# Kernel tuning notes

Measured on AMD Instinct MI355X. Metric: run time of the kernel, lower is better.

## Reference

```python
import jax, jax.numpy as jnp
import numpy as np

GRID = (32, 32)
LATENT = 256
ALPHA = 1.0
DECAY = 0.9


def _cdist(a, b):
    # Euclidean pairwise distance with a grad-safe sqrt (0 where d2==0, like torch.cdist).
    d2 = jnp.sum(a * a, -1)[:, None] + jnp.sum(b * b, -1)[None, :] - 2.0 * (a @ b.T)
    d2 = jnp.maximum(d2, 0.0)
    mask = d2 > 0
    return jnp.where(mask, jnp.sqrt(jnp.where(mask, d2, 1.0)), 0.0)


def setup_inputs() -> dict:
    key = jax.random.key(0)
    k1, k2 = jax.random.split(key)
    z = jax.random.normal(k1, (64, 512, 256), dtype=jnp.float32)
    nodes = jax.random.normal(k2, (GRID[0], GRID[1], LATENT), dtype=jnp.float32)
    return {"z": z, "nodes": nodes}


def reference(z, nodes):
    b, t, d = z.shape
    # time_decay^(seq_len - t - 1)
    tw = DECAY ** (t - 1 - jnp.arange(t, dtype=jnp.float32))
    z_flat = (z * tw[None, :, None]).reshape(b * t, d)   # (b t) d
    nodes_flat = nodes.reshape(-1, d)                     # n d

    dist = _cdist(z_flat, nodes_flat)                     # (b t) n
    q = 1.0 / (1.0 + dist / ALPHA) ** ((ALPHA + 1.0) / 2.0)
    q = q / jnp.sum(q, axis=-1, keepdims=True)            # L1 normalize rows
    q2 = q * q
    p = q2 / jnp.sum(q2, axis=0, keepdims=True)
    p = p / jnp.sum(p, axis=-1, keepdims=True)

    bmu = jnp.argmin(dist, axis=-1).reshape(b, t)         # int32

    # F.kl_div(q.log(), p, reduction='batchmean') = sum(p*(log p - log q)) / N
    kl_loss = jnp.sum(p * (jnp.log(p) - jnp.log(q))) / (b * t)
    diversity_loss = -jnp.mean(_cdist(nodes_flat, nodes_flat))
    time_smooth_loss = jnp.mean((z[:, 1:] - z[:, :-1]) ** 2) * DECAY

    # vectorized neighborhood consistency (python loop in the original is an
    # unweighted mean over all (b, t) adjacent pairs since seq_len is uniform)
    gw = GRID[1]
    pc = jnp.stack([bmu[:, :-1] // gw, bmu[:, :-1] % gw], axis=-1)
    nc = jnp.stack([bmu[:, 1:] // gw, bmu[:, 1:] % gw], axis=-1)
    neighbor_loss = jnp.mean(jnp.sum(jnp.abs(pc - nc), axis=-1).astype(jnp.float32))

    total_loss = kl_loss + 0.5 * diversity_loss + 0.3 * time_smooth_loss + 0.2 * neighbor_loss

    bmu_nodes = nodes_flat[bmu.reshape(-1)].reshape(b, t, d)
    som_z = z + 0.1 * (bmu_nodes - z)
    return (som_z, total_loss, kl_loss, diversity_loss, time_smooth_loss, neighbor_loss, q, bmu)
```

## Files before the change

kernel.cpp:

```cpp
#include <hip/hip_runtime.h>
#include <math.h>

#define Bb 64
#define Tt 512
#define Dd 256
#define Nn 1024
#define NROWS 32768

#define OUT_SOM 0L
#define OUT_SCAL 8388608L
#define OUT_Q 8388613L
#define OUT_BMU 41943045L

typedef __attribute__((ext_vector_type(8))) short bf16x8;
typedef __attribute__((ext_vector_type(4))) float f32x4;
typedef unsigned long long u64;
typedef unsigned short ushortT;

static __device__ __forceinline__ unsigned short f2bf(float x) {
  unsigned int u = __float_as_uint(x);
  unsigned int r = (u + 0x7fffu + ((u >> 16) & 1u)) >> 16;
  return (unsigned short)r;
}
static __device__ __forceinline__ float bf2f(unsigned short b) {
  return __uint_as_float(((unsigned int)b) << 16);
}

static __device__ __forceinline__ float block_reduce_sum(float v, float* sb) {
#pragma unroll
  for (int o = 32; o > 0; o >>= 1) v += __shfl_down(v, o, 64);
  const int lane = threadIdx.x & 63, w = threadIdx.x >> 6;
  if (lane == 0) sb[w] = v;
  __syncthreads();
  return (threadIdx.x == 0) ? (sb[0] + sb[1] + sb[2] + sb[3]) : 0.0f;
}

__global__ __launch_bounds__(256) void k_conv(
    const float* __restrict__ z, const float* __restrict__ nodes,
    ushortT* __restrict__ zhiF, ushortT* __restrict__ zloF, float* __restrict__ zn,
    ushortT* __restrict__ nhiF, ushortT* __restrict__ nloF, float* __restrict__ nnorm) {
  __shared__ float sm[32 * 260];
  const int tid = threadIdx.x;
  if (blockIdx.x < 1024) {
    const int rt = blockIdx.x;
    const long row0 = (long)rt * 32;
    const int r = tid >> 3, c8 = tid & 7;
    const long rowg = row0 + r;
    const int t = (int)(rowg & (Tt - 1));
    const float tw = powf(0.9f, (float)(Tt - 1 - t));
    float nrm = 0.f;
#pragma unroll
    for (int k = 0; k < 8; ++k) {
      const int c4 = c8 + k * 8;
      float4 v = ((const float4*)(z + rowg * Dd))[c4];
      v.x *= tw; v.y *= tw; v.z *= tw; v.w *= tw;
      *(float4*)&sm[r * 260 + c4 * 4] = v;
      nrm += v.x * v.x + v.y * v.y + v.z * v.z + v.w * v.w;
    }
    nrm += __shfl_xor(nrm, 1, 64);
    nrm += __shfl_xor(nrm, 2, 64);
    nrm += __shfl_xor(nrm, 4, 64);
    if (c8 == 0) zn[rowg] = nrm;
    __syncthreads();
    ushort4* oh = (ushort4*)(zhiF + (long)rt * 8192);
    ushort4* ol = (ushort4*)(zloF + (long)rt * 8192);
#pragma unroll
    for (int i = 0; i < 8; ++i) {
      const int o4 = tid + 256 * i;
      const int e4 = (o4 & 1) * 4;
      const int r16 = (o4 >> 1) & 15;
      const int k8 = (o4 >> 5) & 3;
      const int g = (o4 >> 7) & 1;
      const int ks = o4 >> 8;
      const float* p = &sm[(g * 16 + r16) * 260 + ks * 32 + k8 * 8 + e4];
      const float4 v = *(const float4*)p;
      ushort4 h, l;
      h.x = f2bf(v.x); l.x = f2bf(v.x - bf2f(h.x));
      h.y = f2bf(v.y); l.y = f2bf(v.y - bf2f(h.y));
      h.z = f2bf(v.z); l.z = f2bf(v.z - bf2f(h.z));
      h.w = f2bf(v.w); l.w = f2bf(v.w - bf2f(h.w));
      oh[o4] = h;
      ol[o4] = l;
    }
  } else {
    const int ct = blockIdx.x - 1024;
    const int jr = tid >> 4, cg = tid & 15;
    const long nrow = (long)(ct * 16 + jr);
    float nrm = 0.f;
#pragma unroll
    for (int k = 0; k < 4; ++k) {
      const int c4 = cg + k * 16;
      const float4 v = ((const float4*)(nodes + nrow * Dd))[c4];
      *(float4*)&sm[jr * 260 + c4 * 4] = v;
      nrm += v.x * v.x + v.y * v.y + v.z * v.z + v.w * v.w;
    }
    nrm += __shfl_xor(nrm, 1, 64);
    nrm += __shfl_xor(nrm, 2, 64);
    nrm += __shfl_xor(nrm, 4, 64);
    nrm += __shfl_xor(nrm, 8, 64);
    if (cg == 0) nnorm[nrow] = nrm;
    __syncthreads();
    ushort4* oh = (ushort4*)(nhiF + (long)ct * 4096);
    ushort4* ol = (ushort4*)(nloF + (long)ct * 4096);
#pragma unroll
    for (int i = 0; i < 4; ++i) {
      const int o4 = tid + 256 * i;
      const int e4 = (o4 & 1) * 4;
      const int c16 = (o4 >> 1) & 15;
      const int k8 = (o4 >> 5) & 3;
      const int ks = o4 >> 7;
      const float* p = &sm[c16 * 260 + ks * 32 + k8 * 8 + e4];
      const float4 v = *(const float4*)p;
      ushort4 h, l;
      h.x = f2bf(v.x); l.x = f2bf(v.x - bf2f(h.x));
      h.y = f2bf(v.y); l.y = f2bf(v.y - bf2f(h.y));
      h.z = f2bf(v.z); l.z = f2bf(v.z - bf2f(h.z));
      h.w = f2bf(v.w); l.w = f2bf(v.w - bf2f(h.w));
      oh[o4] = h;
      ol[o4] = l;
    }
  }
}

__global__ __launch_bounds__(1024, 4) void k_gemm4(
    const ushortT* __restrict__ zhiF, const ushortT* __restrict__ zloF,
    const ushortT* __restrict__ nhiF, const ushortT* __restrict__ nloF,
    const float* __restrict__ zn, const float* __restrict__ nn,
    float* __restrict__ qout, float* __restrict__ bmuf, float* __restrict__ colsum) {
  __shared__ float srowS[32][16];
  __shared__ u64 sbmu[32][16];
  __shared__ float sinv[32];
  const int tid = threadIdx.x, lane = tid & 63, w = tid >> 6;
  const int rl = lane & 15, kq = lane >> 4;
  const int rt = blockIdx.x;
  const long row0 = (long)rt * 32;

  const ushortT* Ah = zhiF + (long)rt * 8192;
  const ushortT* Al = zloF + (long)rt * 8192;
  const ushortT* Bh = nhiF + (long)w * 4 * 4096;
  const ushortT* Bl = nloF + (long)w * 4 * 4096;
  const int lo8 = lane * 8;

  f32x4 acc[2][4];
#pragma unroll
  for (int g = 0; g < 2; ++g)
#pragma unroll
    for (int c = 0; c < 4; ++c) acc[g][c] = (f32x4){0.f, 0.f, 0.f, 0.f};

#pragma unroll 2
  for (int ks = 0; ks < 8; ++ks) {
    bf16x8 ah[2], al[2], bh[4], bl[4];
#pragma unroll
    for (int g = 0; g < 2; ++g) {
      ah[g] = *(const bf16x8*)(Ah + (ks * 2 + g) * 512 + lo8);
      al[g] = *(const bf16x8*)(Al + (ks * 2 + g) * 512 + lo8);
    }
#pragma unroll
    for (int c = 0; c < 4; ++c) {
      bh[c] = *(const bf16x8*)(Bh + c * 4096 + ks * 512 + lo8);
      bl[c] = *(const bf16x8*)(Bl + c * 4096 + ks * 512 + lo8);
    }
    __builtin_amdgcn_s_setprio(1);
#pragma unroll
    for (int c = 0; c < 4; ++c)
#pragma unroll
      for (int g = 0; g < 2; ++g) {
        acc[g][c] = __builtin_amdgcn_mfma_f32_16x16x32_bf16(ah[g], bh[c], acc[g][c], 0, 0, 0);
        acc[g][c] = __builtin_amdgcn_mfma_f32_16x16x32_bf16(ah[g], bl[c], acc[g][c], 0, 0, 0);
        acc[g][c] = __builtin_amdgcn_mfma_f32_16x16x32_bf16(al[g], bh[c], acc[g][c], 0, 0, 0);
      }
    __builtin_amdgcn_s_setprio(0);
  }

  float nnv[4];
#pragma unroll
  for (int c = 0; c < 4; ++c) nnv[c] = nn[w * 64 + c * 16 + rl];

  float rs[2][4];
  u64 bm[2][4];
#pragma unroll
  for (int g = 0; g < 2; ++g)
#pragma unroll
    for (int r = 0; r < 4; ++r) {
      rs[g][r] = 0.f;
      bm[g][r] = ~0ull;
    }
#pragma unroll
  for (int g = 0; g < 2; ++g) {
    float znv[4];
#pragma unroll
    for (int r = 0; r < 4; ++r) znv[r] = zn[row0 + g * 16 + kq * 4 + r];
#pragma unroll
    for (int c = 0; c < 4; ++c)
#pragma unroll
      for (int r = 0; r < 4; ++r) {
        const float dot = acc[g][c][r];
        const float d2 = znv[r] + nnv[c] - 2.f * dot;
        const float dist = sqrtf(fmaxf(d2, 0.f));
        const float qv = 1.f / (1.f + dist);
        acc[g][c][r] = qv;
        rs[g][r] += qv;
        const int col = w * 64 + c * 16 + rl;
        const u64 pk = ((u64)__float_as_uint(dist) << 32) | (unsigned int)col;
        bm[g][r] = pk < bm[g][r] ? pk : bm[g][r];
      }
  }
#pragma unroll
  for (int g = 0; g < 2; ++g)
#pragma unroll
    for (int r = 0; r < 4; ++r) {
#pragma unroll
      for (int m = 1; m < 16; m <<= 1) {
        rs[g][r] += __shfl_xor(rs[g][r], m, 64);
        const u64 o = __shfl_xor(bm[g][r], m, 64);
        bm[g][r] = o < bm[g][r] ? o : bm[g][r];
      }
      if (rl == 0) {
        srowS[g * 16 + kq * 4 + r][w] = rs[g][r];
        sbmu[g * 16 + kq * 4 + r][w] = bm[g][r];
      }
    }
  __syncthreads();
  if (tid < 32) {
    float s = 0.f;
    u64 best = ~0ull;
#pragma unroll
    for (int i = 0; i < 16; ++i) {
      s += srowS[tid][i];
      const u64 v = sbmu[tid][i];
      best = v < best ? v : best;
    }
    sinv[tid] = 1.f / s;
    bmuf[row0 + tid] = (float)(int)(unsigned int)(best & 0xffffffffull);
  }
  __syncthreads();

  float cp[4];
#pragma unroll
  for (int c = 0; c < 4; ++c) cp[c] = 0.f;
#pragma unroll
  for (int g = 0; g < 2; ++g) {
    float inv[4];
#pragma unroll
    for (int r = 0; r < 4; ++r) inv[r] = sinv[g * 16 + kq * 4 + r];
#pragma unroll
    for (int c = 0; c < 4; ++c)
#pragma unroll
      for (int r = 0; r < 4; ++r) {
        const float qn = acc[g][c][r] * inv[r];
        qout[(row0 + g * 16 + kq * 4 + r) * Nn + w * 64 + c * 16 + rl] = qn;
        cp[c] = fmaf(qn, qn, cp[c]);
      }
  }
#pragma unroll
  for (int c = 0; c < 4; ++c) {
    cp[c] += __shfl_xor(cp[c], 16, 64);
    cp[c] += __shfl_xor(cp[c], 32, 64);
    if (kq == 0) atomicAdd(&colsum[w * 64 + c * 16 + rl], cp[c]);
  }
}

__global__ __launch_bounds__(256) void k_div2(
    const ushortT* __restrict__ nhiF, const ushortT* __restrict__ nloF,
    const float* __restrict__ nnorm, float* __restrict__ scal) {
  __shared__ float sb[4];
  const int tid = threadIdx.x, lane = tid & 63, w = tid >> 6;
  const int rl = lane & 15, kq = lane >> 4;
  const int bi = blockIdx.x & 63;
  const int cq = blockIdx.x >> 6;
  const int lo8 = lane * 8;

  f32x4 acc[4];
#pragma unroll
  for (int c = 0; c < 4; ++c) acc[c] = (f32x4){0.f, 0.f, 0.f, 0.f};

#pragma unroll 2
  for (int ks = 0; ks < 8; ++ks) {
    const bf16x8 ah = *(const bf16x8*)(nhiF + (long)bi * 4096 + ks * 512 + lo8);
    const bf16x8 al = *(const bf16x8*)(nloF + (long)bi * 4096 + ks * 512 + lo8);
#pragma unroll
    for (int c = 0; c < 4; ++c) {
      const long ct = (long)(cq * 16 + w * 4 + c);
      const bf16x8 bh = *(const bf16x8*)(nhiF + ct * 4096 + ks * 512 + lo8);
      const bf16x8 bl = *(const bf16x8*)(nloF + ct * 4096 + ks * 512 + lo8);
      acc[c] = __builtin_amdgcn_mfma_f32_16x16x32_bf16(ah, bh, acc[c], 0, 0, 0);
      acc[c] = __builtin_amdgcn_mfma_f32_16x16x32_bf16(ah, bl, acc[c], 0, 0, 0);
      acc[c] = __builtin_amdgcn_mfma_f32_16x16x32_bf16(al, bh, acc[c], 0, 0, 0);
    }
  }
  float ni[4];
#pragma unroll
  for (int r = 0; r < 4; ++r) ni[r] = nnorm[bi * 16 + kq * 4 + r];
  float dsum = 0.f;
#pragma unroll
  for (int c = 0; c < 4; ++c) {
    const float nj = nnorm[(cq * 16 + w * 4 + c) * 16 + rl];
#pragma unroll
    for (int r = 0; r < 4; ++r) {
      const float d2 = ni[r] + nj - 2.f * acc[c][r];
      dsum += sqrtf(fmaxf(d2, 0.f));
    }
  }
  const float tot = block_reduce_sum(dsum, sb);
  if (tid == 0) atomicAdd(&scal[1], tot);
}

__global__ __launch_bounds__(256) void k_kl(const float* __restrict__ q,
                                            const float* __restrict__ colsum,
                                            float* __restrict__ scal) {
  __shared__ float4 rcs4[Nn / 4];
  __shared__ float4 lcs4[Nn / 4];
  __shared__ float sb[4];
  const int tid = threadIdx.x, lane = tid & 63, wave = tid >> 6;
  {
    const float c0 = colsum[tid * 4 + 0];
    const float c1 = colsum[tid * 4 + 1];
    const float c2 = colsum[tid * 4 + 2];
    const float c3 = colsum[tid * 4 + 3];
    rcs4[tid] = make_float4(1.f / c0, 1.f / c1, 1.f / c2, 1.f / c3);
    lcs4[tid] = make_float4(__logf(c0), __logf(c1), __logf(c2), __logf(c3));
  }
  __syncthreads();
  const long r0 = (long)blockIdx.x * 16;
  float klp = 0.f;
  for (int rr = 0; rr < 4; ++rr) {
    const long row = r0 + rr * 4 + wave;
    float s = 0.f, a = 0.f;
#pragma unroll
    for (int j = 0; j < 4; ++j) {
      const int c4 = lane + 64 * j;
      const float4 qv = *(const float4*)(q + row * Nn + c4 * 4);
      const float4 rc = rcs4[c4];
      const float4 lc = lcs4[c4];
      float u;
      u = qv.x * qv.x * rc.x; s += u; a = fmaf(u, __logf(qv.x) - lc.x, a);
      u = qv.y * qv.y * rc.y; s += u; a = fmaf(u, __logf(qv.y) - lc.y, a);
      u = qv.z * qv.z * rc.z; s += u; a = fmaf(u, __logf(qv.z) - lc.z, a);
      u = qv.w * qv.w * rc.w; s += u; a = fmaf(u, __logf(qv.w) - lc.w, a);
    }
#pragma unroll
    for (int o = 1; o < 64; o <<= 1) {
      s += __shfl_xor(s, o, 64);
      a += __shfl_xor(a, o, 64);
    }
    if (lane == 0) klp += a / s - __logf(s);
  }
  const float tot = block_reduce_sum(klp, sb);
  if (tid == 0) atomicAdd(&scal[0], tot);
}

__global__ __launch_bounds__(256) void k_somnb(const float* __restrict__ z,
                                               const float* __restrict__ nodes,
                                               const float* __restrict__ bmuf,
                                               float* __restrict__ som,
                                               float* __restrict__ scal) {
  __shared__ float sb[4];
  const int tid = threadIdx.x;
  const long r0 = (long)blockIdx.x * 16;
  float ts = 0.f, zp = 0.f;
  if ((r0 & (Tt - 1)) > 0) zp = z[(r0 - 1) * Dd + tid];
  for (int r = 0; r < 16; ++r) {
    const long row = r0 + r;
    const float zc = z[row * Dd + tid];
    const int bi = (int)bmuf[row];
    const float nv = nodes[(long)bi * Dd + tid];
    som[row * Dd + tid] = zc + 0.1f * (nv - zc);
    if ((row & (Tt - 1)) > 0) {
      const float dd = zc - zp;
      ts = fmaf(dd, dd, ts);
    }
    zp = zc;
  }
  const float tts = block_reduce_sum(ts, sb);
  if (tid == 0) atomicAdd(&scal[2], tts);
  float nbv = 0.f;
  if (tid < 16) {
    const long row = r0 + tid;
    if ((row & (Tt - 1)) != (Tt - 1)) {
      const int b1 = (int)bmuf[row], b2 = (int)bmuf[row + 1];
      nbv = (float)(abs((b1 >> 5) - (b2 >> 5)) + abs((b1 & 31) - (b2 & 31)));
    }
  }
  __syncthreads();
  const float tnb = block_reduce_sum(nbv, sb);
  if (tid == 0) atomicAdd(&scal[3], tnb);
}

__global__ void k_final(const float* __restrict__ scal, float* __restrict__ o) {
  const float kl = scal[0] * (1.f / 32768.f);
  const float dv = -scal[1] * (1.f / (1024.f * 1024.f));
  const float ts = scal[2] * (0.9f / (64.f * 511.f * 256.f));
  const float nb = scal[3] * (1.f / 32704.f);
  o[0] = kl + 0.5f * dv + 0.3f * ts + 0.2f * nb;
  o[1] = kl;
  o[2] = dv;
  o[3] = ts;
  o[4] = nb;
}

__global__ __launch_bounds__(256) void k_prep_fb(const float* __restrict__ nodes,
                                                 float* __restrict__ nt,
                                                 float* __restrict__ nnorm) {
  __shared__ float sb[4];
  const int j = blockIdx.x, d = threadIdx.x;
  const float v = nodes[j * Dd + d];
  nt[(long)d * Nn + j] = v;
  const float tot = block_reduce_sum(v * v, sb);
  if (threadIdx.x == 0) nnorm[j] = tot;
}

__global__ __launch_bounds__(256) void k_div_fb(const float* __restrict__ nodes,
                                                const float* __restrict__ nt,
                                                const float* __restrict__ nnorm,
                                                float* __restrict__ scal) {
  __shared__ float ni[4][Dd];
  __shared__ float sb[4];
  const int tid = threadIdx.x;
  const int i0 = blockIdx.x * 4;
#pragma unroll
  for (int r = 0; r < 4; ++r) ni[r][tid] = nodes[(i0 + r) * Dd + tid];
  __syncthreads();
  float acc[4][4];
#pragma unroll
  for (int r = 0; r < 4; ++r)
#pragma unroll
    for (int jj = 0; jj < 4; ++jj) acc[r][jj] = 0.f;
  for (int d = 0; d < Dd; ++d) {
    float nj[4];
#pragma unroll
    for (int jj = 0; jj < 4; ++jj) nj[jj] = nt[(long)d * Nn + tid + 256 * jj];
#pragma unroll
    for (int r = 0; r < 4; ++r) {
      const float s = ni[r][d];
#pragma unroll
      for (int jj = 0; jj < 4; ++jj) acc[r][jj] = fmaf(s, nj[jj], acc[r][jj]);
    }
  }
  float sum = 0.f;
#pragma unroll
  for (int r = 0; r < 4; ++r)
#pragma unroll
    for (int jj = 0; jj < 4; ++jj) {
      const float d2 = nnorm[i0 + r] + nnorm[tid + 256 * jj] - 2.f * acc[r][jj];
      sum += sqrtf(fmaxf(d2, 0.f));
    }
  const float tot = block_reduce_sum(sum, sb);
  if (tid == 0) atomicAdd(&scal[1], tot);
}

__global__ __launch_bounds__(256) void k_dist_fb(
    const float* __restrict__ z, const float* __restrict__ nt,
    const float* __restrict__ nnorm, float* __restrict__ qout,
    float* __restrict__ srow, float* __restrict__ bmuf) {
  __shared__ float zt[Dd][65];
  __shared__ float rs4[4][64];
  __shared__ u64 cand[4][64];
  const int tid = threadIdx.x, lane = tid & 63, wave = tid >> 6;
  const long row0 = (long)blockIdx.x * 64;
  for (int k = 0; k < 64; ++k) {
    const int t = (int)((row0 + k) & (Tt - 1));
    const float tw = powf(0.9f, (float)(Tt - 1 - t));
    zt[tid][k] = z[(row0 + k) * Dd + tid] * tw;
  }
  __syncthreads();
  float zns = 0.f;
  for (int d = 0; d < Dd; ++d) {
    const float v = zt[d][lane];
    zns = fmaf(v, v, zns);
  }
  const long myrow = row0 + lane;
  float rsum = 0.f;
  u64 best = ~0ull;
  const int j0w = wave * 256;
  for (int chunk = 0; chunk < 16; ++chunk) {
    const int j0 = j0w + chunk * 16;
    float acc[16];
#pragma unroll
    for (int i = 0; i < 16; ++i) acc[i] = 0.f;
    const float* ntp = nt + j0;
    for (int d = 0; d < Dd; ++d) {
      const float zv = zt[d][lane];
      const float4 a = ((const float4*)ntp)[0];
      const float4 b = ((const float4*)ntp)[1];
      const float4 c = ((const float4*)ntp)[2];
      const float4 e = ((const float4*)ntp)[3];
      ntp += Nn;
      acc[0] = fmaf(zv, a.x, acc[0]); acc[1] = fmaf(zv, a.y, acc[1]);
      acc[2] = fmaf(zv, a.z, acc[2]); acc[3] = fmaf(zv, a.w, acc[3]);
      acc[4] = fmaf(zv, b.x, acc[4]); acc[5] = fmaf(zv, b.y, acc[5]);
      acc[6] = fmaf(zv, b.z, acc[6]); acc[7] = fmaf(zv, b.w, acc[7]);
      acc[8] = fmaf(zv, c.x, acc[8]); acc[9] = fmaf(zv, c.y, acc[9]);
      acc[10] = fmaf(zv, c.z, acc[10]); acc[11] = fmaf(zv, c.w, acc[11]);
      acc[12] = fmaf(zv, e.x, acc[12]); acc[13] = fmaf(zv, e.y, acc[13]);
      acc[14] = fmaf(zv, e.z, acc[14]); acc[15] = fmaf(zv, e.w, acc[15]);
    }
#pragma unroll
    for (int jj = 0; jj < 16; ++jj) {
      const int j = j0 + jj;
      const float d2 = zns + nnorm[j] - 2.f * acc[jj];
      const float dist = sqrtf(fmaxf(d2, 0.f));
      const float qr = 1.f / (1.f + dist);
      qout[myrow * Nn + j] = qr;
      rsum += qr;
      const u64 pk = ((u64)__float_as_uint(dist) << 32) | (unsigned int)j;
      best = pk < best ? pk : best;
    }
  }
  rs4[wave][lane] = rsum;
  cand[wave][lane] = best;
  __syncthreads();
  if (wave == 0) {
    const float s = rs4[0][lane] + rs4[1][lane] + rs4[2][lane] + rs4[3][lane];
    srow[myrow] = s;
    const u64 m0 = cand[0][lane] < cand[1][lane] ? cand[0][lane] : cand[1][lane];
    const u64 m1 = cand[2][lane] < cand[3][lane] ? cand[2][lane] : cand[3][lane];
    const u64 m = m0 < m1 ? m0 : m1;
    bmuf[myrow] = (float)(int)(unsigned int)(m & 0xffffffffull);
  }
}

__global__ __launch_bounds__(256) void k_norm_fb(float* __restrict__ q,
                                                 const float* __restrict__ srow,
                                                 float* __restrict__ colsum) {
  const int tid = threadIdx.x;
  const long r0 = (long)blockIdx.x * 16;
  float cs[4] = {0.f, 0.f, 0.f, 0.f};
  for (int r = 0; r < 16; ++r) {
    const long row = r0 + r;
    const float inv = 1.f / srow[row];
#pragma unroll
    for (int j = 0; j < 4; ++j) {
      const long idx = row * Nn + tid + 256 * j;
      const float v = q[idx] * inv;
      q[idx] = v;
      cs[j] = fmaf(v, v, cs[j]);
    }
  }
#pragma unroll
  for (int j = 0; j < 4; ++j) atomicAdd(&colsum[tid + 256 * j], cs[j]);
}

extern "C" void kernel_launch(void* const* d_in, const int* in_sizes, int n_in,
                              void* d_out, int out_size, void* d_ws, size_t ws_size,
                              hipStream_t stream) {
  const float* z = (const float*)d_in[0];
  const float* nodes = (const float*)d_in[1];
  float* out = (float*)d_out;
  unsigned char* ws = (unsigned char*)d_ws;

  float* som = out + OUT_SOM;
  float* scal_out = out + OUT_SCAL;
  float* qout = out + OUT_Q;
  float* bmuf = out + OUT_BMU;

  const size_t NEED = 34742288;
  if (ws_size >= NEED) {
    ushortT* zhiF = (ushortT*)(ws + 0);
    ushortT* zloF = (ushortT*)(ws + 16777216);
    ushortT* nhiF = (ushortT*)(ws + 33554432);
    ushortT* nloF = (ushortT*)(ws + 34078720);
    float* zn = (float*)(ws + 34603008);
    float* nnorm = (float*)(ws + 34734080);
    float* colsum = (float*)(ws + 34738176);
    float* scal = (float*)(ws + 34742272);

    hipMemsetAsync(colsum, 0, 4096 + 16, stream);

    k_conv<<<1088, 256, 0, stream>>>(z, nodes, zhiF, zloF, zn, nhiF, nloF, nnorm);
    k_gemm4<<<1024, 1024, 0, stream>>>(zhiF, zloF, nhiF, nloF, zn, nnorm, qout, bmuf, colsum);
    k_div2<<<256, 256, 0, stream>>>(nhiF, nloF, nnorm, scal);
    k_kl<<<2048, 256, 0, stream>>>(qout, colsum, scal);
    k_somnb<<<2048, 256, 0, stream>>>(z, nodes, bmuf, som, scal);
    k_final<<<1, 1, 0, stream>>>(scal, scal_out);
  } else {
    float* wsf = (float*)ws;
    float* nt = wsf;
    float* nnorm = wsf + 262144;
    float* srow = wsf + 263168;
    float* colsum = wsf + 295936;
    float* scal = wsf + 296960;

    hipMemsetAsync(colsum, 0, (1024 + 4) * sizeof(float), stream);
    k_prep_fb<<<1024, 256, 0, stream>>>(nodes, nt, nnorm);
    k_div_fb<<<256, 256, 0, stream>>>(nodes, nt, nnorm, scal);
    k_dist_fb<<<512, 256, 0, stream>>>(z, nt, nnorm, qout, srow, bmuf);
    k_norm_fb<<<2048, 256, 0, stream>>>(qout, srow, colsum);
    k_kl<<<2048, 256, 0, stream>>>(qout, colsum, scal);
    k_somnb<<<2048, 256, 0, stream>>>(z, nodes, bmuf, som, scal);
    k_final<<<1, 1, 0, stream>>>(scal, scal_out);
  }
}
```

Measured before the change: 251.6 us.

## Stage A tile in LDS via direct loads and double-buffer B fragments

The GEMM kernel now copies each block's shared 32-row z hi/lo tile into LDS with global_load_lds, so the 16 waves no longer each fetch it from global memory. The K loop is fully unrolled and the node (B) fragments are double-buffered in registers, so the next step's loads are issued before the current step's MFMAs. This is meant to cut redundant global traffic and hide load latency behind the MFMAs, at the cost of 32KB of LDS per block, more VGPRs, and possible lower occupancy.

```diff
diff --git a/kernel.cpp b/kernel.cpp
--- a/kernel.cpp
+++ b/kernel.cpp
@@ -122,11 +122,36 @@
   }
 }
 
-__global__ __launch_bounds__(1024, 4) void k_gemm4(
+#define KSTEP(KS, CURH, CURL, NXTH, NXTL, PRELOAD)                                             \
+  {                                                                                            \
+    if (PRELOAD) {                                                                             \
+      _Pragma("unroll") for (int c = 0; c < 4; ++c) {                                          \
+        NXTH[c] = *(const bf16x8*)(Bh + c * 4096 + (KS + 1) * 512);                            \
+        NXTL[c] = *(const bf16x8*)(Bl + c * 4096 + (KS + 1) * 512);                            \
+      }                                                                                        \
+    }                                                                                          \
+    const bf16x8 ah0 = *(const bf16x8*)(sA + (KS * 2 + 0) * 512 + lo8);                        \
+    const bf16x8 ah1 = *(const bf16x8*)(sA + (KS * 2 + 1) * 512 + lo8);                        \
+    const bf16x8 al0 = *(const bf16x8*)(sA + 8192 + (KS * 2 + 0) * 512 + lo8);                 \
+    const bf16x8 al1 = *(const bf16x8*)(sA + 8192 + (KS * 2 + 1) * 512 + lo8);                 \
+    __builtin_amdgcn_s_setprio(1);                                                             \
+    _Pragma("unroll") for (int c = 0; c < 4; ++c) {                                            \
+      acc[0][c] = __builtin_amdgcn_mfma_f32_16x16x32_bf16(ah0, CURH[c], acc[0][c], 0, 0, 0);   \
+      acc[0][c] = __builtin_amdgcn_mfma_f32_16x16x32_bf16(ah0, CURL[c], acc[0][c], 0, 0, 0);   \
+      acc[0][c] = __builtin_amdgcn_mfma_f32_16x16x32_bf16(al0, CURH[c], acc[0][c], 0, 0, 0);   \
+      acc[1][c] = __builtin_amdgcn_mfma_f32_16x16x32_bf16(ah1, CURH[c], acc[1][c], 0, 0, 0);   \
+      acc[1][c] = __builtin_amdgcn_mfma_f32_16x16x32_bf16(ah1, CURL[c], acc[1][c], 0, 0, 0);   \
+      acc[1][c] = __builtin_amdgcn_mfma_f32_16x16x32_bf16(al1, CURH[c], acc[1][c], 0, 0, 0);   \
+    }                                                                                          \
+    __builtin_amdgcn_s_setprio(0);                                                             \
+  }
+
+__global__ __launch_bounds__(1024, 4) void k_gemm5(
     const ushortT* __restrict__ zhiF, const ushortT* __restrict__ zloF,
     const ushortT* __restrict__ nhiF, const ushortT* __restrict__ nloF,
     const float* __restrict__ zn, const float* __restrict__ nn,
     float* __restrict__ qout, float* __restrict__ bmuf, float* __restrict__ colsum) {
+  __shared__ __align__(16) ushortT sA[16384];
   __shared__ float srowS[32][16];
   __shared__ u64 sbmu[32][16];
   __shared__ float sinv[32];
@@ -134,43 +159,44 @@
   const int rl = lane & 15, kq = lane >> 4;
   const int rt = blockIdx.x;
   const long row0 = (long)rt * 32;
-
-  const ushortT* Ah = zhiF + (long)rt * 8192;
-  const ushortT* Al = zloF + (long)rt * 8192;
-  const ushortT* Bh = nhiF + (long)w * 4 * 4096;
-  const ushortT* Bl = nloF + (long)w * 4 * 4096;
   const int lo8 = lane * 8;
 
+  {
+    const ushortT* srcH = zhiF + (long)rt * 8192 + tid * 8;
+    const ushortT* srcL = zloF + (long)rt * 8192 + tid * 8;
+    __builtin_amdgcn_global_load_lds(
+        (const __attribute__((address_space(1))) void*)srcH,
+        (__attribute__((address_space(3))) void*)(sA + w * 512), 16, 0, 0);
+    __builtin_amdgcn_global_load_lds(
+        (const __attribute__((address_space(1))) void*)srcL,
+        (__attribute__((address_space(3))) void*)(sA + 8192 + w * 512), 16, 0, 0);
+  }
+
+  const ushortT* Bh = nhiF + (long)w * 4 * 4096 + lo8;
+  const ushortT* Bl = nloF + (long)w * 4 * 4096 + lo8;
+
   f32x4 acc[2][4];
 #pragma unroll
   for (int g = 0; g < 2; ++g)
 #pragma unroll
     for (int c = 0; c < 4; ++c) acc[g][c] = (f32x4){0.f, 0.f, 0.f, 0.f};
 
-#pragma unroll 2
-  for (int ks = 0; ks < 8; ++ks) {
-    bf16x8 ah[2], al[2], bh[4], bl[4];
-#pragma unroll
-    for (int g = 0; g < 2; ++g) {
-      ah[g] = *(const bf16x8*)(Ah + (ks * 2 + g) * 512 + lo8);
-      al[g] = *(const bf16x8*)(Al + (ks * 2 + g) * 512 + lo8);
-    }
-#pragma unroll
-    for (int c = 0; c < 4; ++c) {
-      bh[c] = *(const bf16x8*)(Bh + c * 4096 + ks * 512 + lo8);
-      bl[c] = *(const bf16x8*)(Bl + c * 4096 + ks * 512 + lo8);
-    }
-    __builtin_amdgcn_s_setprio(1);
-#pragma unroll
-    for (int c = 0; c < 4; ++c)
-#pragma unroll
-      for (int g = 0; g < 2; ++g) {
-        acc[g][c] = __builtin_amdgcn_mfma_f32_16x16x32_bf16(ah[g], bh[c], acc[g][c], 0, 0, 0);
-        acc[g][c] = __builtin_amdgcn_mfma_f32_16x16x32_bf16(ah[g], bl[c], acc[g][c], 0, 0, 0);
-        acc[g][c] = __builtin_amdgcn_mfma_f32_16x16x32_bf16(al[g], bh[c], acc[g][c], 0, 0, 0);
-      }
-    __builtin_amdgcn_s_setprio(0);
-  }
+  bf16x8 b0h[4], b0l[4], b1h[4], b1l[4];
+#pragma unroll
+  for (int c = 0; c < 4; ++c) {
+    b0h[c] = *(const bf16x8*)(Bh + c * 4096);
+    b0l[c] = *(const bf16x8*)(Bl + c * 4096);
+  }
+  __syncthreads();
+
+  KSTEP(0, b0h, b0l, b1h, b1l, true)
+  KSTEP(1, b1h, b1l, b0h, b0l, true)
+  KSTEP(2, b0h, b0l, b1h, b1l, true)
+  KSTEP(3, b1h, b1l, b0h, b0l, true)
+  KSTEP(4, b0h, b0l, b1h, b1l, true)
+  KSTEP(5, b1h, b1l, b0h, b0l, true)
+  KSTEP(6, b0h, b0l, b1h, b1l, true)
+  KSTEP(7, b1h, b1l, b0h, b0l, false)
 
   float nnv[4];
 #pragma unroll
@@ -567,7 +593,7 @@
     hipMemsetAsync(colsum, 0, 4096 + 16, stream);
 
     k_conv<<<1088, 256, 0, stream>>>(z, nodes, zhiF, zloF, zn, nhiF, nloF, nnorm);
-    k_gemm4<<<1024, 1024, 0, stream>>>(zhiF, zloF, nhiF, nloF, zn, nnorm, qout, bmuf, colsum);
+    k_gemm5<<<1024, 1024, 0, stream>>>(zhiF, zloF, nhiF, nloF, zn, nnorm, qout, bmuf, colsum);
     k_div2<<<256, 256, 0, stream>>>(nhiF, nloF, nnorm, scal);
     k_kl<<<2048, 256, 0, stream>>>(qout, colsum, scal);
     k_somnb<<<2048, 256, 0, stream>>>(z, nodes, bmuf, som, scal);
```

New measurement: 272.0 us. 8.1% more time.
